# Optimization experiments

Measured on AMD Instinct MI355X. Metric: run time of the kernel, lower is better.

## Reference

```python
import jax, jax.numpy as jnp
import numpy as np

REG_MAX = 16


def _yolo_losses(cls_preds, reg_preds, targets):
    # targets: [B, N, 5] = (class_id, x1, y1, x2, y2); class_id < 0 -> invalid
    mask = targets[..., 0] >= 0.0                      # [B, N]
    cid = jnp.maximum(targets[..., 0], 0.0).astype(jnp.int32)
    x1, y1, x2, y2 = (targets[..., k] for k in (1, 2, 3, 4))
    cx = (x1 + x2) * 0.5
    cy = (y1 + y2) * 0.5
    nvalid = mask.astype(cls_preds[0].dtype).sum(-1)   # [B] valid targets per image
    cls_l = jnp.float32(0.0)
    box_l = jnp.float32(0.0)
    dfl_l = jnp.float32(0.0)
    for i, (cp, rp) in enumerate(zip(cls_preds, reg_preds)):
        B, nc, H, W = cp.shape
        s = 8.0 * (2 ** i)                             # stride of this FPN level
        # int() truncation == floor for positive coords, then clamp (as in torch)
        gx = jnp.clip((cx / s).astype(jnp.int32), 0, W - 1)   # [B, N]
        gy = jnp.clip((cy / s).astype(jnp.int32), 0, H - 1)
        # Faithful to torch's cls_pred_b.view(-1, nc): row r of the CE input is
        # the r-th contiguous nc-chunk of the flattened [C,H,W] tensor.
        logits = cp.reshape(B, H * W, nc)
        lse = jax.nn.logsumexp(logits, axis=-1)        # [B, HW]
        base = jnp.mean(lse - logits[..., 0], axis=-1) # CE when every row label is 0
        bi = jnp.arange(B)[:, None]
        t = gy * W + gx                                # row whose label becomes cid
        adj = (logits[bi, t, 0] - logits[bi, t, cid]) / (H * W)  # [B, N]
        # original recomputes full-grid CE once PER target -> n_valid * base + adj
        cls_l = cls_l + jnp.sum(base * nvalid) + jnp.sum(jnp.where(mask, adj, 0.0))
        pred = rp[bi, :, gy, gx].reshape(B, -1, 4, REG_MAX)      # [B, N, 4, reg_max]
        tx = (cx - gx.astype(cx.dtype) * s) / s
        ty = (cy - gy.astype(cy.dtype) * s) / s
        treg = jnp.stack([tx, ty, (x2 - x1) / s, (y2 - y1) / s], axis=-1)  # [B,N,4]
        box_per = jnp.mean(jnp.abs(pred.mean(-1) - treg), axis=-1)         # [B,N]
        dfl_per = jnp.mean(jnp.abs(pred - treg[..., None]), axis=(-2, -1)) # [B,N]
        box_l = box_l + jnp.sum(jnp.where(mask, box_per, 0.0))
        dfl_l = dfl_l + jnp.sum(jnp.where(mask, dfl_per, 0.0))
    total = 0.3 * cls_l + 8.0 * box_l + 1.5 * dfl_l
    return total, cls_l, box_l, dfl_l


def setup_inputs() -> dict:
    key = jax.random.key(0)
    B, N, NC, RM = 32, 64, 4, REG_MAX
    IMG = 1024.0
    ks = jax.random.split(key, 13)
    sizes = [128, 64, 32, 16]  # strides 8, 16, 32, 64 on a 1024px image
    inp = {}
    for j, hw in enumerate(sizes):
        inp[f"cls_p{j + 3}"] = jax.random.normal(ks[j], (B, NC, hw, hw), jnp.float32)
        inp[f"reg_p{j + 3}"] = jax.random.normal(ks[4 + j], (B, 4 * RM, hw, hw), jnp.float32)
    cx = jax.random.uniform(ks[8], (B, N), minval=64.0, maxval=IMG - 64.0)
    cy = jax.random.uniform(ks[9], (B, N), minval=64.0, maxval=IMG - 64.0)
    w = jax.random.uniform(ks[10], (B, N), minval=8.0, maxval=128.0)
    h = jax.random.uniform(ks[11], (B, N), minval=8.0, maxval=128.0)
    cid = jax.random.randint(ks[12], (B, N), 0, NC).astype(jnp.float32)
    inp["targets"] = jnp.stack(
        [cid, cx - w / 2, cy - h / 2, cx + w / 2, cy + h / 2], axis=-1
    )
    return inp


def reference(cls_p3, cls_p4, cls_p5, cls_p6, reg_p3, reg_p4, reg_p5, reg_p6, targets):
    cls_preds = [cls_p3, cls_p4, cls_p5, cls_p6]
    reg_preds = [reg_p3, reg_p4, reg_p5, reg_p6]
    total, cls_l, box_l, dfl_l = _yolo_losses(cls_preds, reg_preds, targets)
    return total, cls_l, box_l, dfl_l
```

## Files before the change

kernel.cpp:

```cpp
#include <hip/hip_runtime.h>
#include <math.h>


__device__ inline float waveReduceSum(float v) {
#pragma unroll
    for (int m = 32; m >= 1; m >>= 1) v += __shfl_xor(v, m, 64);
    return v;
}

__global__ __launch_bounds__(256) void target_kernel(
    const float* __restrict__ c0, const float* __restrict__ c1,
    const float* __restrict__ c2, const float* __restrict__ c3,
    const float* __restrict__ r0, const float* __restrict__ r1,
    const float* __restrict__ r2, const float* __restrict__ r3,
    const float* __restrict__ tgt, float* __restrict__ ws)
{
    int lvl = blockIdx.x >> 7;
    int rem = blockIdx.x & 127;
    int b   = rem >> 2;
    int g   = rem & 3;

    int tid = threadIdx.x;
    int n_local = tid >> 4;
    int d = (tid >> 2) & 3;
    int q = tid & 3;
    int n = g * 16 + n_local;

    const float* T = tgt + (b * 64 + n) * 5;
    float t0 = T[0], x1 = T[1], y1 = T[2], x2 = T[3], y2 = T[4];
    bool mask = t0 >= 0.f;

    float cx = (x1 + x2) * 0.5f, cy = (y1 + y2) * 0.5f;
    int Wl = 128 >> lvl;
    int HW = Wl * Wl;
    float s = (float)(8 << lvl);
    float invs = 1.f / s;
    int gx = (int)(cx * invs); gx = min(max(gx, 0), Wl - 1);
    int gy = (int)(cy * invs); gy = min(max(gy, 0), Wl - 1);
    int cid = (int)fmaxf(t0, 0.f); cid = min(max(cid, 0), 3);

    const float* cp; const float* rp;
    if (lvl == 0)      { cp = c0; rp = r0; }
    else if (lvl == 1) { cp = c1; rp = r1; }
    else if (lvl == 2) { cp = c2; rp = r2; }
    else               { cp = c3; rp = r3; }

    int t = gy * Wl + gx;

    float tx = (cx - (float)gx * s) * invs;
    float ty = (cy - (float)gy * s) * invs;
    float tr = (d == 0) ? tx : (d == 1) ? ty
             : (d == 2) ? (x2 - x1) * invs : (y2 - y1) * invs;

    const float* rb = rp + ((size_t)b * 64 * HW + t);
    float v0 = rb[(size_t)(d * 16 + q * 4 + 0) * HW];
    float v1 = rb[(size_t)(d * 16 + q * 4 + 1) * HW];
    float v2 = rb[(size_t)(d * 16 + q * 4 + 2) * HW];
    float v3 = rb[(size_t)(d * 16 + q * 4 + 3) * HW];

    float s4 = v0 + v1 + v2 + v3;
    float dfl_c = fabsf(v0 - tr) + fabsf(v1 - tr) +
                  fabsf(v2 - tr) + fabsf(v3 - tr);
    float s8  = s4 + __shfl_xor(s4, 1, 64);
    float s16 = s8 + __shfl_xor(s8, 2, 64);

    float box_c = 0.f, adj_c = 0.f, nv_c = 0.f;
    if (q == 0) {
        box_c = fabsf(s16 * (1.f / 16.f) - tr) * 0.25f;
        if (d == 0) {
            const float* cb = cp + ((size_t)b * 4 * HW + 4 * t);
            adj_c = (cb[0] - cb[cid]) / (float)HW;
            nv_c = mask ? 1.f : 0.f;
        }
    }
    if (!mask) { adj_c = 0.f; box_c = 0.f; dfl_c = 0.f; }
    dfl_c *= (1.f / 64.f);

    float ra = waveReduceSum(adj_c);
    float rbx = waveReduceSum(box_c);
    float rd = waveReduceSum(dfl_c);
    float rn = waveReduceSum(nv_c);
    __shared__ float red[4][4];
    int lane = tid & 63, wid = tid >> 6;
    if (lane == 0) { red[wid][0] = ra; red[wid][1] = rbx;
                     red[wid][2] = rd; red[wid][3] = rn; }
    __syncthreads();
    if (tid == 0) {
        atomicAdd(&ws[33], red[0][0] + red[1][0] + red[2][0] + red[3][0]);
        atomicAdd(&ws[34], red[0][1] + red[1][1] + red[2][1] + red[3][1]);
        atomicAdd(&ws[35], red[0][2] + red[1][2] + red[2][2] + red[3][2]);
        if (lvl == 0)
            atomicAdd(&ws[b], red[0][3] + red[1][3] + red[2][3] + red[3][3]);
    }
}

__global__ __launch_bounds__(256) void base_kernel(
    const float* __restrict__ c0, const float* __restrict__ c1,
    const float* __restrict__ c2, const float* __restrict__ c3,
    const float* __restrict__ nvalid, float* __restrict__ partials)
{
    constexpr int E0 = 32 * 16384;
    constexpr int E1 = E0 + 32 * 4096;
    constexpr int E2 = E1 + 32 * 1024;
    constexpr int E3 = E2 + 32 * 256;

    float acc = 0.f;
    int stride = gridDim.x * 256;
    for (int c = blockIdx.x * 256 + threadIdx.x; c < E3; c += stride) {
        const float* p; int local; int lg; float invHW;
        if (c < E0)      { p = c0; local = c;      lg = 14; invHW = 1.f / 16384.f; }
        else if (c < E1) { p = c1; local = c - E0; lg = 12; invHW = 1.f / 4096.f; }
        else if (c < E2) { p = c2; local = c - E1; lg = 10; invHW = 1.f / 1024.f; }
        else             { p = c3; local = c - E2; lg = 8;  invHW = 1.f / 256.f; }
        float4 v = ((const float4*)p)[local];
        float mx = fmaxf(fmaxf(v.x, v.y), fmaxf(v.z, v.w));
        float lse = logf(expf(v.x - mx) + expf(v.y - mx) +
                         expf(v.z - mx) + expf(v.w - mx)) + mx;
        acc += (lse - v.x) * nvalid[local >> lg] * invHW;
    }

    float w = waveReduceSum(acc);
    __shared__ float red[4];
    int lane = threadIdx.x & 63, wid = threadIdx.x >> 6;
    if (lane == 0) red[wid] = w;
    __syncthreads();
    if (threadIdx.x == 0)
        partials[blockIdx.x] = red[0] + red[1] + red[2] + red[3];
}

__global__ __launch_bounds__(256) void finalize_kernel(
    const float* __restrict__ ws, const float* __restrict__ partials,
    int np, float* __restrict__ out)
{
    float acc = 0.f;
    for (int i = threadIdx.x; i < np; i += 256) acc += partials[i];
    float w = waveReduceSum(acc);
    __shared__ float red[4];
    int lane = threadIdx.x & 63, wid = threadIdx.x >> 6;
    if (lane == 0) red[wid] = w;
    __syncthreads();
    if (threadIdx.x == 0) {
        float base = red[0] + red[1] + red[2] + red[3];
        float cls = base + ws[33];
        float box = ws[34];
        float dfl = ws[35];
        out[0] = 0.3f * cls + 8.f * box + 1.5f * dfl;
        out[1] = cls;
        out[2] = box;
        out[3] = dfl;
    }
}

extern "C" void kernel_launch(void* const* d_in, const int* in_sizes, int n_in,
                              void* d_out, int out_size, void* d_ws, size_t ws_size,
                              hipStream_t stream) {
    const float* c0 = (const float*)d_in[0];
    const float* r0 = (const float*)d_in[1];
    const float* c1 = (const float*)d_in[2];
    const float* r1 = (const float*)d_in[3];
    const float* c2 = (const float*)d_in[4];
    const float* r2 = (const float*)d_in[5];
    const float* c3 = (const float*)d_in[6];
    const float* r3 = (const float*)d_in[7];
    const float* tgt = (const float*)d_in[8];
    float* ws = (float*)d_ws;
    float* out = (float*)d_out;

    constexpr int K1_BLOCKS = 1024;

    hipMemsetAsync(d_ws, 0, 36 * sizeof(float), stream);
    target_kernel<<<512, 256, 0, stream>>>(c0, c1, c2, c3, r0, r1, r2, r3, tgt, ws);
    base_kernel<<<K1_BLOCKS, 256, 0, stream>>>(c0, c1, c2, c3, ws, ws + 36);
    finalize_kernel<<<1, 256, 0, stream>>>(ws, ws + 36, K1_BLOCKS, out);
}
```

Measured before the change: 236.5 us.

## Fuse target and base kernels into one launch, drop memset and atomics

Merges the per-target gather kernel and the full-grid logsumexp kernel into a single launch, with block ranges dispatched to either role. Each base block recomputes the per-image valid-target counts locally, so the memset and the atomics that produced them are no longer needed. All partial sums go into per-block float4 slots that one finalize kernel reduces, which removes two launches and the atomic contention. The base work now runs on 256 blocks instead of 1024, so each thread does more grid-stride iterations and each base block adds a redundant 2048-element target scan.

```diff
diff --git a/kernel.cpp b/kernel.cpp
--- a/kernel.cpp
+++ b/kernel.cpp
@@ -1,6 +1,10 @@
 #include <hip/hip_runtime.h>
 #include <math.h>
 
+
+#define TGT_BLOCKS 512
+#define BASE_BLOCKS 256
+#define NBLK (TGT_BLOCKS + BASE_BLOCKS)
 
 __device__ inline float waveReduceSum(float v) {
 #pragma unroll
@@ -8,142 +12,150 @@
     return v;
 }
 
-__global__ __launch_bounds__(256) void target_kernel(
+__global__ __launch_bounds__(256) void fused_kernel(
     const float* __restrict__ c0, const float* __restrict__ c1,
     const float* __restrict__ c2, const float* __restrict__ c3,
     const float* __restrict__ r0, const float* __restrict__ r1,
     const float* __restrict__ r2, const float* __restrict__ r3,
-    const float* __restrict__ tgt, float* __restrict__ ws)
+    const float* __restrict__ tgt, float4* __restrict__ partials)
 {
-    int lvl = blockIdx.x >> 7;
-    int rem = blockIdx.x & 127;
-    int b   = rem >> 2;
-    int g   = rem & 3;
+    int tid = threadIdx.x;
+    float4 part = make_float4(0.f, 0.f, 0.f, 0.f);
 
-    int tid = threadIdx.x;
-    int n_local = tid >> 4;
-    int d = (tid >> 2) & 3;
-    int q = tid & 3;
-    int n = g * 16 + n_local;
+    if (blockIdx.x < TGT_BLOCKS) {
+        int lvl = blockIdx.x >> 7;
+        int rem = blockIdx.x & 127;
+        int b   = rem >> 2;
+        int g   = rem & 3;
+        int n_local = tid >> 4;
+        int d = (tid >> 2) & 3;
+        int q = tid & 3;
+        int n = g * 16 + n_local;
 
-    const float* T = tgt + (b * 64 + n) * 5;
-    float t0 = T[0], x1 = T[1], y1 = T[2], x2 = T[3], y2 = T[4];
-    bool mask = t0 >= 0.f;
+        const float* T = tgt + (b * 64 + n) * 5;
+        float t0 = T[0], x1 = T[1], y1 = T[2], x2 = T[3], y2 = T[4];
+        bool mask = t0 >= 0.f;
 
-    float cx = (x1 + x2) * 0.5f, cy = (y1 + y2) * 0.5f;
-    int Wl = 128 >> lvl;
-    int HW = Wl * Wl;
-    float s = (float)(8 << lvl);
-    float invs = 1.f / s;
-    int gx = (int)(cx * invs); gx = min(max(gx, 0), Wl - 1);
-    int gy = (int)(cy * invs); gy = min(max(gy, 0), Wl - 1);
-    int cid = (int)fmaxf(t0, 0.f); cid = min(max(cid, 0), 3);
+        float cx = (x1 + x2) * 0.5f, cy = (y1 + y2) * 0.5f;
+        int Wl = 128 >> lvl;
+        int HW = Wl * Wl;
+        float s = (float)(8 << lvl);
+        float invs = 1.f / s;
+        int gx = (int)(cx * invs); gx = min(max(gx, 0), Wl - 1);
+        int gy = (int)(cy * invs); gy = min(max(gy, 0), Wl - 1);
+        int cid = (int)fmaxf(t0, 0.f); cid = min(max(cid, 0), 3);
 
-    const float* cp; const float* rp;
-    if (lvl == 0)      { cp = c0; rp = r0; }
-    else if (lvl == 1) { cp = c1; rp = r1; }
-    else if (lvl == 2) { cp = c2; rp = r2; }
-    else               { cp = c3; rp = r3; }
+        const float* cp; const float* rp;
+        if (lvl == 0)      { cp = c0; rp = r0; }
+        else if (lvl == 1) { cp = c1; rp = r1; }
+        else if (lvl == 2) { cp = c2; rp = r2; }
+        else               { cp = c3; rp = r3; }
 
-    int t = gy * Wl + gx;
+        int t = gy * Wl + gx;
+        float tx = (cx - (float)gx * s) * invs;
+        float ty = (cy - (float)gy * s) * invs;
+        float tr = (d == 0) ? tx : (d == 1) ? ty
+                 : (d == 2) ? (x2 - x1) * invs : (y2 - y1) * invs;
 
-    float tx = (cx - (float)gx * s) * invs;
-    float ty = (cy - (float)gy * s) * invs;
-    float tr = (d == 0) ? tx : (d == 1) ? ty
-             : (d == 2) ? (x2 - x1) * invs : (y2 - y1) * invs;
+        const float* rb = rp + ((size_t)b * 64 * HW + t);
+        float v0 = rb[(size_t)(d * 16 + q * 4 + 0) * HW];
+        float v1 = rb[(size_t)(d * 16 + q * 4 + 1) * HW];
+        float v2 = rb[(size_t)(d * 16 + q * 4 + 2) * HW];
+        float v3 = rb[(size_t)(d * 16 + q * 4 + 3) * HW];
 
-    const float* rb = rp + ((size_t)b * 64 * HW + t);
-    float v0 = rb[(size_t)(d * 16 + q * 4 + 0) * HW];
-    float v1 = rb[(size_t)(d * 16 + q * 4 + 1) * HW];
-    float v2 = rb[(size_t)(d * 16 + q * 4 + 2) * HW];
-    float v3 = rb[(size_t)(d * 16 + q * 4 + 3) * HW];
+        float s4 = v0 + v1 + v2 + v3;
+        float dfl_c = fabsf(v0 - tr) + fabsf(v1 - tr) +
+                      fabsf(v2 - tr) + fabsf(v3 - tr);
+        float s8  = s4 + __shfl_xor(s4, 1, 64);
+        float s16 = s8 + __shfl_xor(s8, 2, 64);
 
-    float s4 = v0 + v1 + v2 + v3;
-    float dfl_c = fabsf(v0 - tr) + fabsf(v1 - tr) +
-                  fabsf(v2 - tr) + fabsf(v3 - tr);
-    float s8  = s4 + __shfl_xor(s4, 1, 64);
-    float s16 = s8 + __shfl_xor(s8, 2, 64);
+        float box_c = 0.f, adj_c = 0.f;
+        if (q == 0) {
+            box_c = fabsf(s16 * (1.f / 16.f) - tr) * 0.25f;
+            if (d == 0) {
+                const float* cb = cp + ((size_t)b * 4 * HW + 4 * t);
+                adj_c = (cb[0] - cb[cid]) / (float)HW;
+            }
+        }
+        if (!mask) { adj_c = 0.f; box_c = 0.f; dfl_c = 0.f; }
+        dfl_c *= (1.f / 64.f);
 
-    float box_c = 0.f, adj_c = 0.f, nv_c = 0.f;
-    if (q == 0) {
-        box_c = fabsf(s16 * (1.f / 16.f) - tr) * 0.25f;
-        if (d == 0) {
-            const float* cb = cp + ((size_t)b * 4 * HW + 4 * t);
-            adj_c = (cb[0] - cb[cid]) / (float)HW;
-            nv_c = mask ? 1.f : 0.f;
+        part.y = waveReduceSum(adj_c);
+        part.z = waveReduceSum(box_c);
+        part.w = waveReduceSum(dfl_c);
+    } else {
+        __shared__ float nv[32];
+        {
+            int c = 0;
+#pragma unroll
+            for (int k = 0; k < 8; ++k)
+                c += (tgt[(tid * 8 + k) * 5] >= 0.f) ? 1 : 0;
+            float f = (float)c;
+            f += __shfl_xor(f, 1, 64);
+            f += __shfl_xor(f, 2, 64);
+            f += __shfl_xor(f, 4, 64);
+            if ((tid & 7) == 0) nv[tid >> 3] = f;
         }
+        __syncthreads();
+
+        constexpr int E0 = 32 * 16384;
+        constexpr int E1 = E0 + 32 * 4096;
+        constexpr int E2 = E1 + 32 * 1024;
+        constexpr int E3 = E2 + 32 * 256;
+
+        float acc = 0.f;
+        int stride = BASE_BLOCKS * 256;
+        for (int c = (blockIdx.x - TGT_BLOCKS) * 256 + tid; c < E3; c += stride) {
+            const float* p; int local; int lg; float invHW;
+            if (c < E0)      { p = c0; local = c;      lg = 14; invHW = 1.f / 16384.f; }
+            else if (c < E1) { p = c1; local = c - E0; lg = 12; invHW = 1.f / 4096.f; }
+            else if (c < E2) { p = c2; local = c - E1; lg = 10; invHW = 1.f / 1024.f; }
+            else             { p = c3; local = c - E2; lg = 8;  invHW = 1.f / 256.f; }
+            float4 v = ((const float4*)p)[local];
+            float mx = fmaxf(fmaxf(v.x, v.y), fmaxf(v.z, v.w));
+            float lse = logf(expf(v.x - mx) + expf(v.y - mx) +
+                             expf(v.z - mx) + expf(v.w - mx)) + mx;
+            acc += (lse - v.x) * nv[local >> lg] * invHW;
+        }
+        part.x = waveReduceSum(acc);
     }
-    if (!mask) { adj_c = 0.f; box_c = 0.f; dfl_c = 0.f; }
-    dfl_c *= (1.f / 64.f);
 
-    float ra = waveReduceSum(adj_c);
-    float rbx = waveReduceSum(box_c);
-    float rd = waveReduceSum(dfl_c);
-    float rn = waveReduceSum(nv_c);
-    __shared__ float red[4][4];
+    __shared__ float4 red[4];
     int lane = tid & 63, wid = tid >> 6;
-    if (lane == 0) { red[wid][0] = ra; red[wid][1] = rbx;
-                     red[wid][2] = rd; red[wid][3] = rn; }
+    if (lane == 0) red[wid] = part;
     __syncthreads();
     if (tid == 0) {
-        atomicAdd(&ws[33], red[0][0] + red[1][0] + red[2][0] + red[3][0]);
-        atomicAdd(&ws[34], red[0][1] + red[1][1] + red[2][1] + red[3][1]);
-        atomicAdd(&ws[35], red[0][2] + red[1][2] + red[2][2] + red[3][2]);
-        if (lvl == 0)
-            atomicAdd(&ws[b], red[0][3] + red[1][3] + red[2][3] + red[3][3]);
+        float4 a = red[0], bq = red[1], cq = red[2], dq = red[3];
+        partials[blockIdx.x] = make_float4(a.x + bq.x + cq.x + dq.x,
+                                           a.y + bq.y + cq.y + dq.y,
+                                           a.z + bq.z + cq.z + dq.z,
+                                           a.w + bq.w + cq.w + dq.w);
     }
 }
 
-__global__ __launch_bounds__(256) void base_kernel(
-    const float* __restrict__ c0, const float* __restrict__ c1,
-    const float* __restrict__ c2, const float* __restrict__ c3,
-    const float* __restrict__ nvalid, float* __restrict__ partials)
+__global__ __launch_bounds__(256) void finalize_kernel(
+    const float4* __restrict__ partials, float* __restrict__ out)
 {
-    constexpr int E0 = 32 * 16384;
-    constexpr int E1 = E0 + 32 * 4096;
-    constexpr int E2 = E1 + 32 * 1024;
-    constexpr int E3 = E2 + 32 * 256;
-
-    float acc = 0.f;
-    int stride = gridDim.x * 256;
-    for (int c = blockIdx.x * 256 + threadIdx.x; c < E3; c += stride) {
-        const float* p; int local; int lg; float invHW;
-        if (c < E0)      { p = c0; local = c;      lg = 14; invHW = 1.f / 16384.f; }
-        else if (c < E1) { p = c1; local = c - E0; lg = 12; invHW = 1.f / 4096.f; }
-        else if (c < E2) { p = c2; local = c - E1; lg = 10; invHW = 1.f / 1024.f; }
-        else             { p = c3; local = c - E2; lg = 8;  invHW = 1.f / 256.f; }
-        float4 v = ((const float4*)p)[local];
-        float mx = fmaxf(fmaxf(v.x, v.y), fmaxf(v.z, v.w));
-        float lse = logf(expf(v.x - mx) + expf(v.y - mx) +
-                         expf(v.z - mx) + expf(v.w - mx)) + mx;
-        acc += (lse - v.x) * nvalid[local >> lg] * invHW;
+    int tid = threadIdx.x;
+    float bx = 0.f, by = 0.f, bz = 0.f, bw = 0.f;
+    for (int i = tid; i < NBLK; i += 256) {
+        float4 v = partials[i];
+        bx += v.x; by += v.y; bz += v.z; bw += v.w;
     }
-
-    float w = waveReduceSum(acc);
-    __shared__ float red[4];
-    int lane = threadIdx.x & 63, wid = threadIdx.x >> 6;
-    if (lane == 0) red[wid] = w;
+    bx = waveReduceSum(bx);
+    by = waveReduceSum(by);
+    bz = waveReduceSum(bz);
+    bw = waveReduceSum(bw);
+    __shared__ float4 red[4];
+    int lane = tid & 63, wid = tid >> 6;
+    if (lane == 0) red[wid] = make_float4(bx, by, bz, bw);
     __syncthreads();
-    if (threadIdx.x == 0)
-        partials[blockIdx.x] = red[0] + red[1] + red[2] + red[3];
-}
-
-__global__ __launch_bounds__(256) void finalize_kernel(
-    const float* __restrict__ ws, const float* __restrict__ partials,
-    int np, float* __restrict__ out)
-{
-    float acc = 0.f;
-    for (int i = threadIdx.x; i < np; i += 256) acc += partials[i];
-    float w = waveReduceSum(acc);
-    __shared__ float red[4];
-    int lane = threadIdx.x & 63, wid = threadIdx.x >> 6;
-    if (lane == 0) red[wid] = w;
-    __syncthreads();
-    if (threadIdx.x == 0) {
-        float base = red[0] + red[1] + red[2] + red[3];
-        float cls = base + ws[33];
-        float box = ws[34];
-        float dfl = ws[35];
+    if (tid == 0) {
+        float base = red[0].x + red[1].x + red[2].x + red[3].x;
+        float adj  = red[0].y + red[1].y + red[2].y + red[3].y;
+        float box  = red[0].z + red[1].z + red[2].z + red[3].z;
+        float dfl  = red[0].w + red[1].w + red[2].w + red[3].w;
+        float cls = base + adj;
         out[0] = 0.3f * cls + 8.f * box + 1.5f * dfl;
         out[1] = cls;
         out[2] = box;
@@ -163,13 +175,10 @@
     const float* c3 = (const float*)d_in[6];
     const float* r3 = (const float*)d_in[7];
     const float* tgt = (const float*)d_in[8];
-    float* ws = (float*)d_ws;
+    float4* partials = (float4*)d_ws;
     float* out = (float*)d_out;
 
-    constexpr int K1_BLOCKS = 1024;
-
-    hipMemsetAsync(d_ws, 0, 36 * sizeof(float), stream);
-    target_kernel<<<512, 256, 0, stream>>>(c0, c1, c2, c3, r0, r1, r2, r3, tgt, ws);
-    base_kernel<<<K1_BLOCKS, 256, 0, stream>>>(c0, c1, c2, c3, ws, ws + 36);
-    finalize_kernel<<<1, 256, 0, stream>>>(ws, ws + 36, K1_BLOCKS, out);
+    fused_kernel<<<NBLK, 256, 0, stream>>>(c0, c1, c2, c3, r0, r1, r2, r3,
+                                           tgt, partials);
+    finalize_kernel<<<1, 256, 0, stream>>>(partials, out);
 }
```

Measured after the change: 218.6 us. 1.08x faster.
